# Optimization experiments

Hardware: AMD Instinct MI355X
Metric: run time of the kernel (lower is better)

## Reference

```python
import jax, jax.numpy as jnp
import numpy as np

H = 64          # hidden_size
NG = 5000       # num_genes
B = 32          # num_graphs
N = B * NG      # total nodes
E = 1_600_000   # total edges


def setup_inputs() -> dict:
    key = jax.random.key(0)
    ks = jax.random.split(key, 32)
    def nrm(k, shape, s=0.05):
        return jax.random.normal(k, shape, jnp.float32) * s
    return {
        "x": jax.random.normal(ks[0], (N, 2), jnp.float32),
        "edge_index": jax.random.randint(ks[1], (2, E), 0, N),
        # pert_w: Linear(1, H); gene_basal_w: Linear(1, H)
        "pert_w_W": nrm(ks[2], (H, 1)), "pert_w_b": nrm(ks[3], (H,)),
        "basal_W": nrm(ks[4], (H, 1)), "basal_b": nrm(ks[5], (H,)),
        # gene embedding table (max_norm=True -> rows renormed to norm<=1)
        "emb_table": nrm(ks[6], (NG, H), 0.5),
        # emb_trans: Linear(2H, H)
        "emb_trans_W": nrm(ks[7], (H, 2 * H)), "emb_trans_b": nrm(ks[8], (H,)),
        # pert_base_trans_w: Linear(2H, H)  (gene_pert_agg == 'concat+w')
        "pbt_W": nrm(ks[9], (H, 2 * H)), "pbt_b": nrm(ks[10], (H,)),
        # two GCNConv(H, H) layers
        "gcn1_W": nrm(ks[11], (H, H)), "gcn1_b": nrm(ks[12], (H,)),
        "gcn2_W": nrm(ks[13], (H, H)), "gcn2_b": nrm(ks[14], (H,)),
        # recovery_w: MLP([H, 2H, H, 1]) with BN on first two hidden layers
        "rec_W1": nrm(ks[15], (2 * H, H)), "rec_b1": nrm(ks[16], (2 * H,)),
        "rec_g1": jnp.ones((2 * H,), jnp.float32), "rec_be1": jnp.zeros((2 * H,), jnp.float32),
        "rec_W2": nrm(ks[17], (H, 2 * H)), "rec_b2": nrm(ks[18], (H,)),
        "rec_g2": jnp.ones((H,), jnp.float32), "rec_be2": jnp.zeros((H,), jnp.float32),
        "rec_W3": nrm(ks[19], (1, H)), "rec_b3": nrm(ks[20], (1,)),
    }


def _gcn_conv(h, src, dst, norm, W, b, n_nodes):
    # PyG GCNConv: x' = scatter_add(norm * (x W^T)[src] -> dst) + b, self-loops included in src/dst
    m = h @ W.T                                   # [N, H]
    out = jax.ops.segment_sum(m[src] * norm[:, None], dst, num_segments=n_nodes)
    return out + b


def _batchnorm(z, g, b, eps=1e-5):
    mu = z.mean(0)
    var = z.var(0)
    return (z - mu) * jax.lax.rsqrt(var + eps) * g + b


def reference(x, edge_index, pert_w_W, pert_w_b, basal_W, basal_b, emb_table,
              emb_trans_W, emb_trans_b, pbt_W, pbt_b, gcn1_W, gcn1_b,
              gcn2_W, gcn2_b, rec_W1, rec_b1, rec_g1, rec_be1,
              rec_W2, rec_b2, rec_g2, rec_be2, rec_W3, rec_b3):
    n_nodes = x.shape[0]
    ng = emb_table.shape[0]
    nb = n_nodes // ng

    # GCN normalization with self-loops (computed once, shared by both layers)
    loop = jnp.arange(n_nodes)
    src = jnp.concatenate([edge_index[0], loop])
    dst = jnp.concatenate([edge_index[1], loop])
    deg = jax.ops.segment_sum(jnp.ones_like(src, jnp.float32), dst, num_segments=n_nodes)
    dinv = jnp.where(deg > 0, jax.lax.rsqrt(jnp.maximum(deg, 1.0)), 0.0)
    norm = dinv[src] * dinv[dst]

    pert_emb = x[:, 1:2] @ pert_w_W.T + pert_w_b          # [N, H]
    base = x[:, 0:1] @ basal_W.T + basal_b                # [N, H]

    # nn.Embedding(max_norm=True): renorm rows to max L2 norm of 1
    nrm = jnp.linalg.norm(emb_table, axis=1, keepdims=True)
    emb_n = emb_table * jnp.minimum(1.0, 1.0 / jnp.maximum(nrm, 1e-7))
    emb = jnp.tile(emb_n, (nb, 1))                        # arange(NG).repeat(B) lookup
    base_emb = jnp.concatenate([emb, base], axis=1) @ emb_trans_W.T + emb_trans_b

    def pbt(p, b_):
        return jnp.concatenate([p, b_], axis=1) @ pbt_W.T + pbt_b

    h = pbt(pert_emb, base_emb)
    h = pbt(jax.nn.relu(_gcn_conv(h, src, dst, norm, gcn1_W, gcn1_b, n_nodes)), base_emb)
    h = pbt(jax.nn.relu(_gcn_conv(h, src, dst, norm, gcn2_W, gcn2_b, n_nodes)), base_emb)

    # recovery_w: Linear -> BN -> ReLU -> Linear -> BN -> ReLU -> Linear
    z = jax.nn.relu(_batchnorm(h @ rec_W1.T + rec_b1, rec_g1, rec_be1))
    z = jax.nn.relu(_batchnorm(z @ rec_W2.T + rec_b2, rec_g2, rec_be2))
    out = z @ rec_W3.T + rec_b3                           # [N, 1]
    return out.reshape(nb, ng)
```

## Files before the change

### kernel.cpp

```cpp
#include <hip/hip_runtime.h>


#define GS_GRID 2048
#define GS_BLK  256

enum { A1_=0, A0_=64, C1_=128, C0_=192, D1_=256, D0_=320,
       S1_=384, Q1_=512, SC1_=640, SH1_=768,
       S2_=896, Q2_=960, SC2_=1024, SH2_=1088,
       GD1_=1152, GA1_=1216, G00_=1280,
       GD2_=1344, G02_=1408, RD1_=1472, RD0_=1600, CST_FLOATS=2048 };

__device__ __forceinline__ float wave_sum64(float v) {
#pragma unroll
  for (int o = 32; o; o >>= 1) v += __shfl_xor(v, o, 64);
  return v;
}

__device__ __forceinline__ int rfl(int v) { return __builtin_amdgcn_readfirstlane(v); }

__device__ __forceinline__ float rlane(float v, int k) {
  return __int_as_float(__builtin_amdgcn_readlane(__float_as_int(v), k));
}


__global__ __launch_bounds__(256) void hist_k(const int* __restrict__ ei,
                                              int* __restrict__ hist, int E) {
  __shared__ int h[256];
  const int t = threadIdx.x;
  h[t] = 0;
  __syncthreads();
  const int per = (E + gridDim.x - 1) / gridDim.x;
  const int beg = blockIdx.x * per, end = min(E, beg + per);
  for (int i = beg + t; i < end; i += 256)
    atomicAdd(&h[ei[E + i] >> 10], 1);
  __syncthreads();
  hist[blockIdx.x * 256 + t] = h[t];
}

__global__ void bscan_k(int* __restrict__ hist, int* __restrict__ bucketBase,
                        int* __restrict__ rowptrN, int E, int nblk) {
  const int t = threadIdx.x;
  int run = 0;
  for (int b = 0; b < nblk; ++b) {
    int v = hist[b * 256 + t];
    hist[b * 256 + t] = run;
    run += v;
  }
  __shared__ int sc[256];
  sc[t] = run; __syncthreads();
  for (int o = 1; o < 256; o <<= 1) {
    int x = sc[t]; if (t >= o) x += sc[t - o];
    __syncthreads(); sc[t] = x; __syncthreads();
  }
  bucketBase[t] = sc[t] - run;
  if (t == 255) { bucketBase[256] = sc[t]; rowptrN[0] = E; }
}

__global__ __launch_bounds__(256) void bucket_k(const int* __restrict__ ei,
                                                const int* __restrict__ hist,
                                                const int* __restrict__ bucketBase,
                                                int2* __restrict__ eb, int E) {
  __shared__ int cur[256];
  const int t = threadIdx.x;
  cur[t] = hist[blockIdx.x * 256 + t] + bucketBase[t];
  __syncthreads();
  const int per = (E + gridDim.x - 1) / gridDim.x;
  const int beg = blockIdx.x * per, end = min(E, beg + per);
  for (int i = beg + t; i < end; i += 256) {
    int s = ei[i], d = ei[E + i];
    int pos = atomicAdd(&cur[d >> 10], 1);
    eb[pos] = make_int2(s, d);
  }
}

__global__ __launch_bounds__(256) void csr_k(const int2* __restrict__ eb,
                                             const int* __restrict__ bucketBase,
                                             int* __restrict__ rowptr, float* __restrict__ dinv,
                                             int* __restrict__ col, int N) {
  __shared__ int cnt[1024];
  __shared__ int base[1024];
  __shared__ int red[256];
  const int t = threadIdx.x;
  const int k = blockIdx.x;
  const int nodeBeg = k << 10;
  const int segBeg = bucketBase[k], segEnd = bucketBase[k + 1];
#pragma unroll
  for (int j = t; j < 1024; j += 256) cnt[j] = 0;
  __syncthreads();
  for (int i = segBeg + t; i < segEnd; i += 256)
    atomicAdd(&cnt[eb[i].y & 1023], 1);
  __syncthreads();
  int c0 = cnt[4 * t], c1 = cnt[4 * t + 1], c2 = cnt[4 * t + 2], c3 = cnt[4 * t + 3];
  int ts = c0 + c1 + c2 + c3;
  red[t] = ts; __syncthreads();
  for (int o = 1; o < 256; o <<= 1) {
    int x = red[t]; if (t >= o) x += red[t - o];
    __syncthreads(); red[t] = x; __syncthreads();
  }
  int off = red[t] - ts;
  base[4 * t] = off;
  base[4 * t + 1] = off + c0;
  base[4 * t + 2] = off + c0 + c1;
  base[4 * t + 3] = off + c0 + c1 + c2;
#pragma unroll
  for (int u = 0; u < 4; ++u) {
    int j = 4 * t + u;
    int node = nodeBeg + j;
    if (node < N) {
      rowptr[node] = segBeg + base[j];
      dinv[node] = rsqrtf((float)(cnt[j] + 1));
    }
  }
  __syncthreads();
  cnt[4 * t] = base[4 * t]; cnt[4 * t + 1] = base[4 * t + 1];
  cnt[4 * t + 2] = base[4 * t + 2]; cnt[4 * t + 3] = base[4 * t + 3];
  __syncthreads();
  for (int i = segBeg + t; i < segEnd; i += 256) {
    int2 e = eb[i];
    int pos = atomicAdd(&cnt[e.y & 1023], 1);
    col[segBeg + pos] = e.x;
  }
}

__global__ void consts1_k(const float* __restrict__ pbtW, const float* __restrict__ pertW,
                          const float* __restrict__ pertB, const float* __restrict__ etW,
                          const float* __restrict__ basW, const float* __restrict__ basB,
                          const float* __restrict__ etB, float* __restrict__ cst) {
  int h = threadIdx.x;
  float a1 = 0, a0 = 0, c1 = 0, c0 = 0;
  for (int k = 0; k < 64; ++k) {
    float wp = pbtW[h * 128 + k];
    a1 = fmaf(wp, pertW[k], a1);
    a0 = fmaf(wp, pertB[k], a0);
    float we = etW[h * 128 + 64 + k];
    c1 = fmaf(we, basW[k], c1);
    c0 = fmaf(we, basB[k], c0);
  }
  cst[A1_ + h] = a1; cst[A0_ + h] = a0; cst[C1_ + h] = c1; cst[C0_ + h] = c0 + etB[h];
}

__global__ void consts2_k(const float* __restrict__ pbtW, const float* __restrict__ pbtB,
                          float* __restrict__ cst) {
  int h = threadIdx.x;
  float d1 = 0, d0 = 0;
  for (int k = 0; k < 64; ++k) {
    float w = pbtW[h * 128 + 64 + k];
    d1 = fmaf(w, cst[C1_ + k], d1);
    d0 = fmaf(w, cst[C0_ + k], d0);
  }
  cst[D1_ + h] = d1; cst[D0_ + h] = d0 + pbtB[h];
}

__global__ void consts3_k(const float* __restrict__ g1W, float* __restrict__ cst) {
  int h = threadIdx.x;
  float gd1 = 0, ga1 = 0, g00 = 0;
  for (int k = 0; k < 64; ++k) {
    float w = g1W[h * 64 + k];
    gd1 = fmaf(w, cst[D1_ + k], gd1);
    ga1 = fmaf(w, cst[A1_ + k], ga1);
    g00 = fmaf(w, cst[D0_ + k] + cst[A0_ + k], g00);
  }
  cst[GD1_ + h] = gd1; cst[GA1_ + h] = ga1; cst[G00_ + h] = g00;
}

__global__ void consts5_k(const float* __restrict__ g2W, float* __restrict__ cst) {
  int h = threadIdx.x;
  float a = 0, b = 0;
  for (int k = 0; k < 64; ++k) {
    float w = g2W[h * 64 + k];
    a = fmaf(w, cst[D1_ + k], a);
    b = fmaf(w, cst[D0_ + k], b);
  }
  cst[GD2_ + h] = a; cst[G02_ + h] = b;
}

__global__ void consts6_k(const float* __restrict__ rW1, const float* __restrict__ rb1,
                          float* __restrict__ cst) {
  int c = threadIdx.x;
  float a = 0, b = 0;
  for (int k = 0; k < 64; ++k) {
    float w = rW1[c * 64 + k];
    a = fmaf(w, cst[D1_ + k], a);
    b = fmaf(w, cst[D0_ + k], b);
  }
  cst[RD1_ + c] = a; cst[RD0_ + c] = b + rb1[c];
}

__global__ void constsW_k(const float* __restrict__ g2W, const float* __restrict__ rW1,
                          const float* __restrict__ pbtW,
                          float* __restrict__ Wf, float* __restrict__ Wr) {
  const int t = threadIdx.x;
  for (int e = t; e < 4096; e += 256) {
    int c = e >> 6, j = e & 63;
    float s = 0.f;
    for (int h = 0; h < 64; ++h) s = fmaf(g2W[c * 64 + h], pbtW[h * 128 + j], s);
    Wf[e] = s;
  }
  for (int e = t; e < 8192; e += 256) {
    int c = e >> 6, j = e & 63;
    float s = 0.f;
    for (int h = 0; h < 64; ++h) s = fmaf(rW1[c * 64 + h], pbtW[h * 128 + j], s);
    Wr[e] = s;
  }
}

template <bool NORM>
__global__ __launch_bounds__(256) void geneT_k(const float* __restrict__ in,
                                               const float* __restrict__ W, int ldw,
                                               float* __restrict__ out, int NG) {
  const int lane = threadIdx.x & 63;
  const int wid = blockIdx.x * 4 + (threadIdx.x >> 6);
  const int nw = gridDim.x * 4;
  float w[64];
#pragma unroll
  for (int j = 0; j < 16; ++j) {
    float4 v = *reinterpret_cast<const float4*>(W + lane * ldw + 4 * j);
    w[4 * j] = v.x; w[4 * j + 1] = v.y; w[4 * j + 2] = v.z; w[4 * j + 3] = v.w;
  }
  for (int g = wid; g < NG; g += nw) {
    float e = in[g * 64 + lane];
    if (NORM) {
      float sq = wave_sum64(e * e);
      float nrm = sqrtf(sq);
      float s = nrm > 1.f ? 1.f / nrm : 1.f;
      e *= s;
    }
    float acc = 0.f;
#pragma unroll
    for (int k = 0; k < 64; ++k) acc = fmaf(w[k], rlane(e, k), acc);
    out[g * 64 + lane] = acc;
  }
}

__global__ __launch_bounds__(256) void m1_k(const float* __restrict__ x,
                                            const float* __restrict__ embTm1,
                                            const float* __restrict__ dinv,
                                            const float* __restrict__ cst,
                                            float* __restrict__ m1, int N, int NG) {
  int total = N * 16;
  for (int idx = blockIdx.x * blockDim.x + threadIdx.x; idx < total;
       idx += gridDim.x * blockDim.x) {
    int n = idx >> 4, q = idx & 15;
    int g = n % NG;
    float x0 = x[2 * n], x1 = x[2 * n + 1], dn = dinv[n];
    float4 em = *reinterpret_cast<const float4*>(embTm1 + g * 64 + q * 4);
    float4 gd1 = *reinterpret_cast<const float4*>(cst + GD1_ + q * 4);
    float4 ga1 = *reinterpret_cast<const float4*>(cst + GA1_ + q * 4);
    float4 g00 = *reinterpret_cast<const float4*>(cst + G00_ + q * 4);
    float4 mv;
    mv.x = dn * (fmaf(x0, gd1.x, fmaf(x1, ga1.x, em.x + g00.x)));
    mv.y = dn * (fmaf(x0, gd1.y, fmaf(x1, ga1.y, em.y + g00.y)));
    mv.z = dn * (fmaf(x0, gd1.z, fmaf(x1, ga1.z, em.z + g00.z)));
    mv.w = dn * (fmaf(x0, gd1.w, fmaf(x1, ga1.w, em.w + g00.w)));
    reinterpret_cast<float4*>(m1)[idx] = mv;
  }
}

#define XS_STRIDE 130
#define WS_STRIDE 68
#define OS_STRIDE 68
#define OS_WORDS  (128 * OS_STRIDE)
#define WS_WORDS  (64 * WS_STRIDE)
#define LDS_WORDS (OS_WORDS + WS_WORDS + 128)

template <bool MUL_D, bool STATS>
__global__ __launch_bounds__(256, 4) void gemmt_gv_k(
    const float* __restrict__ in,
    const float* __restrict__ W,
    const float* __restrict__ tbl,
    const float* __restrict__ cA,
    const float* __restrict__ cB,
    const float* __restrict__ x,
    const float* __restrict__ dinv,
    float* __restrict__ out, int ldout,
    float* __restrict__ sums, float* __restrict__ sqs, int N, int NG) {
  __shared__ float lds[LDS_WORDS];
  float* Xs = lds;
  float* Ws = lds + OS_WORDS;
  float* sred = lds + OS_WORDS + WS_WORDS;
  const int t = threadIdx.x;
  const int base = blockIdx.x << 7;
  if (STATS && t < 128) sred[t] = 0.f;

#pragma unroll
  for (int c = 0; c < 16; ++c) {
    int lin = c * 256 + t;
    int cw = lin >> 6, kw = lin & 63;
    Ws[kw * WS_STRIDE + cw] = W[cw * 64 + kw];
  }
#pragma unroll
  for (int c = 0; c < 8; ++c) {
    int lin = c * 256 + t;
    int nl = lin >> 4, k4 = lin & 15;
    int row = base + nl; if (row >= N) row = N - 1;
    float4 v = *reinterpret_cast<const float4*>(in + (size_t)row * 64 + 4 * k4);
    Xs[(4 * k4 + 0) * XS_STRIDE + nl] = v.x;
    Xs[(4 * k4 + 1) * XS_STRIDE + nl] = v.y;
    Xs[(4 * k4 + 2) * XS_STRIDE + nl] = v.z;
    Xs[(4 * k4 + 3) * XS_STRIDE + nl] = v.w;
  }
  __syncthreads();

  const int ng = t & 31;
  const int c0 = (t >> 5) * 8;
  float acc[8][4];
#pragma unroll
  for (int i = 0; i < 8; ++i)
#pragma unroll
    for (int j = 0; j < 4; ++j) acc[i][j] = 0.f;
#pragma unroll 4
  for (int k = 0; k < 64; ++k) {
    float4 wa = *reinterpret_cast<const float4*>(Ws + k * WS_STRIDE + c0);
    float4 wb = *reinterpret_cast<const float4*>(Ws + k * WS_STRIDE + c0 + 4);
    float2 xa = *reinterpret_cast<const float2*>(Xs + k * XS_STRIDE + 2 * ng);
    float2 xb = *reinterpret_cast<const float2*>(Xs + k * XS_STRIDE + 2 * ng + 64);
    const float w8[8] = {wa.x, wa.y, wa.z, wa.w, wb.x, wb.y, wb.z, wb.w};
    const float x4[4] = {xa.x, xa.y, xb.x, xb.y};
#pragma unroll
    for (int ci = 0; ci < 8; ++ci)
#pragma unroll
      for (int xi = 0; xi < 4; ++xi)
        acc[ci][xi] = fmaf(w8[ci], x4[xi], acc[ci][xi]);
  }
  __syncthreads();

  const int nd[4] = {2 * ng, 2 * ng + 1, 2 * ng + 64, 2 * ng + 65};
#pragma unroll
  for (int ci = 0; ci < 8; ++ci) {
    Xs[nd[0] * OS_STRIDE + c0 + ci] = acc[ci][0];
    Xs[nd[1] * OS_STRIDE + c0 + ci] = acc[ci][1];
    Xs[nd[2] * OS_STRIDE + c0 + ci] = acc[ci][2];
    Xs[nd[3] * OS_STRIDE + c0 + ci] = acc[ci][3];
  }
  __syncthreads();

  const int q = t & 15;
  const float4 a4 = *reinterpret_cast<const float4*>(cA + 4 * q);
  const float4 b4 = *reinterpret_cast<const float4*>(cB + 4 * q);
  float4 s4 = make_float4(0.f, 0.f, 0.f, 0.f);
  float4 q4 = make_float4(0.f, 0.f, 0.f, 0.f);
#pragma unroll
  for (int c = 0; c < 8; ++c) {
    int nl = c * 16 + (t >> 4);
    int n = base + nl;
    if (n < N) {
      float4 o = *reinterpret_cast<const float4*>(Xs + nl * OS_STRIDE + 4 * q);
      int g = n % NG;
      float4 tg = *reinterpret_cast<const float4*>(tbl + (size_t)g * 64 + 4 * q);
      float x0 = x[2 * n];
      o.x += fmaf(x0, a4.x, tg.x + b4.x);
      o.y += fmaf(x0, a4.y, tg.y + b4.y);
      o.z += fmaf(x0, a4.z, tg.z + b4.z);
      o.w += fmaf(x0, a4.w, tg.w + b4.w);
      if (MUL_D) {
        float dv = dinv[n];
        o.x *= dv; o.y *= dv; o.z *= dv; o.w *= dv;
      }
      *reinterpret_cast<float4*>(out + (size_t)n * ldout + 4 * q) = o;
      if (STATS) {
        s4.x += o.x; s4.y += o.y; s4.z += o.z; s4.w += o.w;
        q4.x += o.x * o.x; q4.y += o.y * o.y; q4.z += o.z * o.z; q4.w += o.w * o.w;
      }
    }
  }
  if (STATS) {
    atomicAdd(&sred[4 * q + 0], s4.x);
    atomicAdd(&sred[4 * q + 1], s4.y);
    atomicAdd(&sred[4 * q + 2], s4.z);
    atomicAdd(&sred[4 * q + 3], s4.w);
    atomicAdd(&sred[64 + 4 * q + 0], q4.x);
    atomicAdd(&sred[64 + 4 * q + 1], q4.y);
    atomicAdd(&sred[64 + 4 * q + 2], q4.z);
    atomicAdd(&sred[64 + 4 * q + 3], q4.w);
    __syncthreads();
    if (t < 64) {
      atomicAdd(&sums[t], sred[t]);
      atomicAdd(&sqs[t], sred[64 + t]);
    }
  }
}

__global__ __launch_bounds__(256, 4) void gemmt_rec2_k(
    const float* __restrict__ Z,
    const float* __restrict__ W,
    const float* __restrict__ b,
    const float* __restrict__ bnsc, const float* __restrict__ bnsh,
    float* __restrict__ out,
    float* __restrict__ sums, float* __restrict__ sqs, int N) {
  __shared__ float lds[LDS_WORDS];
  float* Xs = lds;
  float* Ws = lds + OS_WORDS;
  float* sred = lds + OS_WORDS + WS_WORDS;
  const int t = threadIdx.x;
  const int base = blockIdx.x << 7;
  if (t < 128) sred[t] = 0.f;

  const int ng = t & 31;
  const int c0 = (t >> 5) * 8;
  float acc[8][4];
#pragma unroll
  for (int i = 0; i < 8; ++i)
#pragma unroll
    for (int j = 0; j < 4; ++j) acc[i][j] = 0.f;

  for (int half = 0; half < 2; ++half) {
    if (half) __syncthreads();
    const int ko = half * 64;
#pragma unroll
    for (int c = 0; c < 16; ++c) {
      int lin = c * 256 + t;
      int cw = lin >> 6, kw = lin & 63;
      Ws[kw * WS_STRIDE + cw] = W[cw * 128 + ko + kw];
    }
#pragma unroll
    for (int c = 0; c < 8; ++c) {
      int lin = c * 256 + t;
      int nl = lin >> 4, k4 = lin & 15;
      int row = base + nl; if (row >= N) row = N - 1;
      float4 v = *reinterpret_cast<const float4*>(Z + (size_t)row * 128 + ko + 4 * k4);
      float4 sc = *reinterpret_cast<const float4*>(bnsc + ko + 4 * k4);
      float4 sh = *reinterpret_cast<const float4*>(bnsh + ko + 4 * k4);
      v.x = fmaxf(fmaf(v.x, sc.x, sh.x), 0.f);
      v.y = fmaxf(fmaf(v.y, sc.y, sh.y), 0.f);
      v.z = fmaxf(fmaf(v.z, sc.z, sh.z), 0.f);
      v.w = fmaxf(fmaf(v.w, sc.w, sh.w), 0.f);
      Xs[(4 * k4 + 0) * XS_STRIDE + nl] = v.x;
      Xs[(4 * k4 + 1) * XS_STRIDE + nl] = v.y;
      Xs[(4 * k4 + 2) * XS_STRIDE + nl] = v.z;
      Xs[(4 * k4 + 3) * XS_STRIDE + nl] = v.w;
    }
    __syncthreads();
#pragma unroll 4
    for (int k = 0; k < 64; ++k) {
      float4 wa = *reinterpret_cast<const float4*>(Ws + k * WS_STRIDE + c0);
      float4 wb = *reinterpret_cast<const float4*>(Ws + k * WS_STRIDE + c0 + 4);
      float2 xa = *reinterpret_cast<const float2*>(Xs + k * XS_STRIDE + 2 * ng);
      float2 xb = *reinterpret_cast<const float2*>(Xs + k * XS_STRIDE + 2 * ng + 64);
      const float w8[8] = {wa.x, wa.y, wa.z, wa.w, wb.x, wb.y, wb.z, wb.w};
      const float x4[4] = {xa.x, xa.y, xb.x, xb.y};
#pragma unroll
      for (int ci = 0; ci < 8; ++ci)
#pragma unroll
        for (int xi = 0; xi < 4; ++xi)
          acc[ci][xi] = fmaf(w8[ci], x4[xi], acc[ci][xi]);
    }
  }
  __syncthreads();

  const int nd[4] = {2 * ng, 2 * ng + 1, 2 * ng + 64, 2 * ng + 65};
#pragma unroll
  for (int ci = 0; ci < 8; ++ci) {
    Xs[nd[0] * OS_STRIDE + c0 + ci] = acc[ci][0];
    Xs[nd[1] * OS_STRIDE + c0 + ci] = acc[ci][1];
    Xs[nd[2] * OS_STRIDE + c0 + ci] = acc[ci][2];
    Xs[nd[3] * OS_STRIDE + c0 + ci] = acc[ci][3];
  }
  __syncthreads();

  const int q = t & 15;
  const float4 bb = *reinterpret_cast<const float4*>(b + 4 * q);
  float4 s4 = make_float4(0.f, 0.f, 0.f, 0.f);
  float4 q4 = make_float4(0.f, 0.f, 0.f, 0.f);
#pragma unroll
  for (int c = 0; c < 8; ++c) {
    int nl = c * 16 + (t >> 4);
    int n = base + nl;
    if (n < N) {
      float4 o = *reinterpret_cast<const float4*>(Xs + nl * OS_STRIDE + 4 * q);
      o.x += bb.x; o.y += bb.y; o.z += bb.z; o.w += bb.w;
      *reinterpret_cast<float4*>(out + (size_t)n * 64 + 4 * q) = o;
      s4.x += o.x; s4.y += o.y; s4.z += o.z; s4.w += o.w;
      q4.x += o.x * o.x; q4.y += o.y * o.y; q4.z += o.z * o.z; q4.w += o.w * o.w;
    }
  }
  atomicAdd(&sred[4 * q + 0], s4.x);
  atomicAdd(&sred[4 * q + 1], s4.y);
  atomicAdd(&sred[4 * q + 2], s4.z);
  atomicAdd(&sred[4 * q + 3], s4.w);
  atomicAdd(&sred[64 + 4 * q + 0], q4.x);
  atomicAdd(&sred[64 + 4 * q + 1], q4.y);
  atomicAdd(&sred[64 + 4 * q + 2], q4.z);
  atomicAdd(&sred[64 + 4 * q + 3], q4.w);
  __syncthreads();
  if (t < 64) {
    atomicAdd(&sums[t], sred[t]);
    atomicAdd(&sqs[t], sred[64 + t]);
  }
}

__global__ __launch_bounds__(256) void gather_k(const float* __restrict__ m,
                                                const int* __restrict__ rowptr,
                                                const int* __restrict__ col,
                                                const float* __restrict__ dinv,
                                                const float* __restrict__ bias,
                                                float* __restrict__ out, int N) {
  const int lane = threadIdx.x & 63;
  const int wid = blockIdx.x * 4 + (threadIdx.x >> 6);
  const int nw = gridDim.x * 4;
  const float b = bias[lane];
  for (int n = wid; n < N; n += nw) {
    const int nn = rfl(n);
    const float dn = dinv[nn];
    float acc = m[(size_t)nn * 64 + lane];
    float acc2 = 0.f;
    const int beg = rfl(rowptr[nn]), end = rfl(rowptr[nn + 1]);
    for (int base = beg; base < end; base += 64) {
      const int rem = end - base;
      const int kk = rem < 64 ? rem : 64;
      int cv = (lane < kk) ? col[base + lane] : 0;
      int k = 0;
      for (; k + 3 < kk; k += 4) {
        int i0 = __shfl(cv, k, 64), i1 = __shfl(cv, k + 1, 64);
        int i2 = __shfl(cv, k + 2, 64), i3 = __shfl(cv, k + 3, 64);
        float v0 = m[(size_t)i0 * 64 + lane];
        float v1 = m[(size_t)i1 * 64 + lane];
        float v2 = m[(size_t)i2 * 64 + lane];
        float v3 = m[(size_t)i3 * 64 + lane];
        acc += v0 + v2; acc2 += v1 + v3;
      }
      for (; k < kk; ++k) acc += m[(size_t)__shfl(cv, k, 64) * 64 + lane];
    }
    out[(size_t)nn * 64 + lane] = fmaxf(fmaf(dn, acc + acc2, b), 0.f);
  }
}

__global__ void bnparam_k(const float* __restrict__ sums, const float* __restrict__ sqs,
                          const float* __restrict__ g, const float* __restrict__ be,
                          float* __restrict__ scale, float* __restrict__ shift, int C,
                          float invN) {
  int t = threadIdx.x;
  if (t < C) {
    float mu = sums[t] * invN;
    float var = fmaxf(sqs[t] * invN - mu * mu, 0.f);
    float sc = g[t] * rsqrtf(var + 1e-5f);
    scale[t] = sc;
    shift[t] = be[t] - mu * sc;
  }
}

__global__ __launch_bounds__(256) void rec3_k(const float* __restrict__ z2,
                                              const float* __restrict__ scale,
                                              const float* __restrict__ shift,
                                              const float* __restrict__ W3,
                                              const float* __restrict__ b3,
                                              float* __restrict__ out, int N) {
  const int lane = threadIdx.x & 63;
  const int wid = blockIdx.x * 4 + (threadIdx.x >> 6);
  const int nw = gridDim.x * 4;
  const float sc = scale[lane], sh = shift[lane], w = W3[lane], b = b3[0];
  for (int n = wid; n < N; n += nw) {
    float v = z2[(size_t)n * 64 + lane];
    v = fmaxf(fmaf(v, sc, sh), 0.f) * w;
    v = wave_sum64(v);
    if (lane == 0) out[n] = v + b;
  }
}

extern "C" void kernel_launch(void* const* d_in, const int* in_sizes, int n_in,
                              void* d_out, int out_size, void* d_ws, size_t ws_size,
                              hipStream_t stream) {
  const float* x     = (const float*)d_in[0];
  const int*   ei    = (const int*)d_in[1];
  const float* pertW = (const float*)d_in[2];
  const float* pertB = (const float*)d_in[3];
  const float* basW  = (const float*)d_in[4];
  const float* basB  = (const float*)d_in[5];
  const float* embTb = (const float*)d_in[6];
  const float* etW   = (const float*)d_in[7];
  const float* etB   = (const float*)d_in[8];
  const float* pbtW  = (const float*)d_in[9];
  const float* pbtB  = (const float*)d_in[10];
  const float* g1W   = (const float*)d_in[11];
  const float* g1B   = (const float*)d_in[12];
  const float* g2W   = (const float*)d_in[13];
  const float* g2B   = (const float*)d_in[14];
  const float* rW1   = (const float*)d_in[15];
  const float* rb1   = (const float*)d_in[16];
  const float* rg1   = (const float*)d_in[17];
  const float* rbe1  = (const float*)d_in[18];
  const float* rW2   = (const float*)d_in[19];
  const float* rb2   = (const float*)d_in[20];
  const float* rg2   = (const float*)d_in[21];
  const float* rbe2  = (const float*)d_in[22];
  const float* rW3   = (const float*)d_in[23];
  const float* rb3   = (const float*)d_in[24];
  float* outp = (float*)d_out;

  const int N  = in_sizes[0] / 2;
  const int E  = in_sizes[1] / 2;
  const int NG = in_sizes[6] / 64;
  const int NB = (N + 1023) >> 10;
  const int NT = (N + 127) >> 7;

  char* p = (char*)d_ws;
  float* cst    = (float*)p; p += CST_FLOATS * 4;
  int*   hist   = (int*)p;   p += 256 * 256 * 4;
  int*   bb     = (int*)p;   p += 1024;
  int*   rowptr = (int*)p;   p += (size_t)(N + 64) * 4;
  float* dinv   = (float*)p; p += (size_t)N * 4;
  int*   col    = (int*)p;   p += (size_t)E * 4;
  float* Wf     = (float*)p; p += 4096 * 4;
  float* Wr     = (float*)p; p += 8192 * 4;
  float* embT   = (float*)p; p += (size_t)NG * 64 * 4;
  float* embT2  = (float*)p; p += (size_t)NG * 64 * 4;
  float* embT2g2= (float*)p; p += (size_t)NG * 64 * 4;
  float* embT2rA= (float*)p; p += (size_t)NG * 64 * 4;
  float* embT2rB= (float*)p; p += (size_t)NG * 64 * 4;
  float* z2buf  = (float*)p; p += (size_t)N * 64 * 4;
  float* hb     = (float*)p; p += (size_t)N * 64 * 4;
  float* tmp1   = (float*)p; p += (size_t)N * 64 * 4;
  float* tmp2   = (float*)p; p += (size_t)N * 64 * 4;
  float* Z = hb;
  float* z2 = z2buf;
  float* embTm1 = embT;
  int2*  eb = (int2*)tmp2;

  dim3 blk(GS_BLK), grid(GS_GRID);

  hipMemsetAsync(cst, 0, CST_FLOATS * 4, stream);

  hist_k<<<256, 256, 0, stream>>>(ei, hist, E);
  bscan_k<<<1, 256, 0, stream>>>(hist, bb, rowptr + N, E, 256);
  bucket_k<<<256, 256, 0, stream>>>(ei, hist, bb, eb, E);
  csr_k<<<NB, 256, 0, stream>>>(eb, bb, rowptr, dinv, col, N);

  consts1_k<<<1, 64, 0, stream>>>(pbtW, pertW, pertB, etW, basW, basB, etB, cst);
  consts2_k<<<1, 64, 0, stream>>>(pbtW, pbtB, cst);
  consts3_k<<<1, 64, 0, stream>>>(g1W, cst);
  consts5_k<<<1, 64, 0, stream>>>(g2W, cst);
  consts6_k<<<1, 128, 0, stream>>>(rW1, rb1, cst);
  constsW_k<<<1, 256, 0, stream>>>(g2W, rW1, pbtW, Wf, Wr);
  geneT_k<true><<<256, 256, 0, stream>>>(embTb, etW, 128, embT, NG);
  geneT_k<false><<<256, 256, 0, stream>>>(embT, pbtW + 64, 128, embT2, NG);
  geneT_k<false><<<256, 256, 0, stream>>>(embT2, g1W, 64, embTm1, NG);
  geneT_k<false><<<256, 256, 0, stream>>>(embT2, g2W, 64, embT2g2, NG);
  geneT_k<false><<<256, 256, 0, stream>>>(embT2, rW1, 64, embT2rA, NG);
  geneT_k<false><<<256, 256, 0, stream>>>(embT2, rW1 + 64 * 64, 64, embT2rB, NG);
  m1_k<<<grid, blk, 0, stream>>>(x, embTm1, dinv, cst, tmp1, N, NG);

  gather_k<<<grid, blk, 0, stream>>>(tmp1, rowptr, col, dinv, g1B, tmp2, N);
  gemmt_gv_k<true, false><<<NT, blk, 0, stream>>>(
      tmp2, Wf, embT2g2, cst + GD2_, cst + G02_, x, dinv, tmp1, 64,
      nullptr, nullptr, N, NG);
  gather_k<<<grid, blk, 0, stream>>>(tmp1, rowptr, col, dinv, g2B, tmp2, N);

  gemmt_gv_k<false, true><<<NT, blk, 0, stream>>>(
      tmp2, Wr, embT2rA, cst + RD1_, cst + RD0_, x, nullptr, Z, 128,
      cst + S1_, cst + Q1_, N, NG);
  gemmt_gv_k<false, true><<<NT, blk, 0, stream>>>(
      tmp2, Wr + 64 * 64, embT2rB, cst + RD1_ + 64, cst + RD0_ + 64, x, nullptr,
      Z + 64, 128, cst + S1_ + 64, cst + Q1_ + 64, N, NG);
  bnparam_k<<<1, 128, 0, stream>>>(cst + S1_, cst + Q1_, rg1, rbe1,
                                   cst + SC1_, cst + SH1_, 128, 1.0f / (float)N);
  gemmt_rec2_k<<<NT, blk, 0, stream>>>(Z, rW2, rb2, cst + SC1_, cst + SH1_,
                                       z2, cst + S2_, cst + Q2_, N);
  bnparam_k<<<1, 64, 0, stream>>>(cst + S2_, cst + Q2_, rg2, rbe2,
                                  cst + SC2_, cst + SH2_, 64, 1.0f / (float)N);
  rec3_k<<<grid, blk, 0, stream>>>(z2, cst + SC2_, cst + SH2_, rW3, rb3, outp, N);
}
```

Baseline: 569.2 us.

## Parallelize bucket scan, fuse rec1 GEMM halves, unroll gather by eight

Replaces the single-block serial histogram scan with a two-stage parallel scan: 256 blocks, each scanning one bucket column, then a small scan over the bucket totals. Merges the two recovery-layer-1 GEMM launches into one kernel that loads the input tile once and computes both 64-column halves with two accumulator sets. Widens the gather inner loop to eight independent loads with four partial sums to expose more memory-level parallelism. The cost is higher register pressure in the fused GEMM and the gather, which may lower occupancy.

Result: faster. 485.9 us (-14.6%).

```diff
diff --git a/kernel.cpp b/kernel.cpp
--- a/kernel.cpp
+++ b/kernel.cpp
@@ -37,22 +37,31 @@
   hist[blockIdx.x * 256 + t] = h[t];
 }
 
-__global__ void bscan_k(int* __restrict__ hist, int* __restrict__ bucketBase,
-                        int* __restrict__ rowptrN, int E, int nblk) {
+__global__ void scan1b_k(int* __restrict__ hist, int* __restrict__ bsum) {
+  __shared__ int sc[256];
   const int t = threadIdx.x;
-  int run = 0;
-  for (int b = 0; b < nblk; ++b) {
-    int v = hist[b * 256 + t];
-    hist[b * 256 + t] = run;
-    run += v;
-  }
-  __shared__ int sc[256];
-  sc[t] = run; __syncthreads();
+  const int b = blockIdx.x;
+  int v = hist[t * 256 + b];
+  sc[t] = v; __syncthreads();
   for (int o = 1; o < 256; o <<= 1) {
     int x = sc[t]; if (t >= o) x += sc[t - o];
     __syncthreads(); sc[t] = x; __syncthreads();
   }
-  bucketBase[t] = sc[t] - run;
+  hist[t * 256 + b] = sc[t] - v;
+  if (t == 255) bsum[b] = sc[t];
+}
+
+__global__ void scan2b_k(const int* __restrict__ bsum, int* __restrict__ bucketBase,
+                         int* __restrict__ rowptrN, int E) {
+  __shared__ int sc[256];
+  const int t = threadIdx.x;
+  int v = bsum[t];
+  sc[t] = v; __syncthreads();
+  for (int o = 1; o < 256; o <<= 1) {
+    int x = sc[t]; if (t >= o) x += sc[t - o];
+    __syncthreads(); sc[t] = x; __syncthreads();
+  }
+  bucketBase[t] = sc[t] - v;
   if (t == 255) { bucketBase[256] = sc[t]; rowptrN[0] = E; }
 }
 
@@ -263,7 +272,7 @@
 #define WS_WORDS  (64 * WS_STRIDE)
 #define LDS_WORDS (OS_WORDS + WS_WORDS + 128)
 
-template <bool MUL_D, bool STATS>
+template <bool MUL_D>
 __global__ __launch_bounds__(256, 4) void gemmt_gv_k(
     const float* __restrict__ in,
     const float* __restrict__ W,
@@ -272,15 +281,12 @@
     const float* __restrict__ cB,
     const float* __restrict__ x,
     const float* __restrict__ dinv,
-    float* __restrict__ out, int ldout,
-    float* __restrict__ sums, float* __restrict__ sqs, int N, int NG) {
+    float* __restrict__ out, int ldout, int N, int NG) {
   __shared__ float lds[LDS_WORDS];
   float* Xs = lds;
   float* Ws = lds + OS_WORDS;
-  float* sred = lds + OS_WORDS + WS_WORDS;
   const int t = threadIdx.x;
   const int base = blockIdx.x << 7;
-  if (STATS && t < 128) sred[t] = 0.f;
 
 #pragma unroll
   for (int c = 0; c < 16; ++c) {
@@ -337,8 +343,6 @@
   const int q = t & 15;
   const float4 a4 = *reinterpret_cast<const float4*>(cA + 4 * q);
   const float4 b4 = *reinterpret_cast<const float4*>(cB + 4 * q);
-  float4 s4 = make_float4(0.f, 0.f, 0.f, 0.f);
-  float4 q4 = make_float4(0.f, 0.f, 0.f, 0.f);
 #pragma unroll
   for (int c = 0; c < 8; ++c) {
     int nl = c * 16 + (t >> 4);
@@ -357,26 +361,181 @@
         o.x *= dv; o.y *= dv; o.z *= dv; o.w *= dv;
       }
       *reinterpret_cast<float4*>(out + (size_t)n * ldout + 4 * q) = o;
-      if (STATS) {
+    }
+  }
+}
+
+__global__ __launch_bounds__(256, 4) void gemmt_rec1_k(
+    const float* __restrict__ in,
+    const float* __restrict__ Wr,
+    const float* __restrict__ tblA, const float* __restrict__ tblB,
+    const float* __restrict__ cA,
+    const float* __restrict__ cB,
+    const float* __restrict__ x,
+    float* __restrict__ Z,
+    float* __restrict__ sums, float* __restrict__ sqs,
+    int N, int NG) {
+  __shared__ float lds[LDS_WORDS];
+  float* Xs = lds;
+  float* Ws = lds + OS_WORDS;
+  float* sred = lds + OS_WORDS + WS_WORDS;
+  const int t = threadIdx.x;
+  const int base = blockIdx.x << 7;
+  if (t < 128) sred[t] = 0.f;
+
+#pragma unroll
+  for (int c = 0; c < 16; ++c) {
+    int lin = c * 256 + t;
+    int cw = lin >> 6, kw = lin & 63;
+    Ws[kw * WS_STRIDE + cw] = Wr[cw * 64 + kw];
+  }
+#pragma unroll
+  for (int c = 0; c < 8; ++c) {
+    int lin = c * 256 + t;
+    int nl = lin >> 4, k4 = lin & 15;
+    int row = base + nl; if (row >= N) row = N - 1;
+    float4 v = *reinterpret_cast<const float4*>(in + (size_t)row * 64 + 4 * k4);
+    Xs[(4 * k4 + 0) * XS_STRIDE + nl] = v.x;
+    Xs[(4 * k4 + 1) * XS_STRIDE + nl] = v.y;
+    Xs[(4 * k4 + 2) * XS_STRIDE + nl] = v.z;
+    Xs[(4 * k4 + 3) * XS_STRIDE + nl] = v.w;
+  }
+  __syncthreads();
+
+  const int ng = t & 31;
+  const int c0 = (t >> 5) * 8;
+  float accA[8][4], accB[8][4];
+#pragma unroll
+  for (int i = 0; i < 8; ++i)
+#pragma unroll
+    for (int j = 0; j < 4; ++j) { accA[i][j] = 0.f; accB[i][j] = 0.f; }
+
+#pragma unroll 4
+  for (int k = 0; k < 64; ++k) {
+    float4 wa = *reinterpret_cast<const float4*>(Ws + k * WS_STRIDE + c0);
+    float4 wb = *reinterpret_cast<const float4*>(Ws + k * WS_STRIDE + c0 + 4);
+    float2 xa = *reinterpret_cast<const float2*>(Xs + k * XS_STRIDE + 2 * ng);
+    float2 xb = *reinterpret_cast<const float2*>(Xs + k * XS_STRIDE + 2 * ng + 64);
+    const float w8[8] = {wa.x, wa.y, wa.z, wa.w, wb.x, wb.y, wb.z, wb.w};
+    const float x4[4] = {xa.x, xa.y, xb.x, xb.y};
+#pragma unroll
+    for (int ci = 0; ci < 8; ++ci)
+#pragma unroll
+      for (int xi = 0; xi < 4; ++xi)
+        accA[ci][xi] = fmaf(w8[ci], x4[xi], accA[ci][xi]);
+  }
+  __syncthreads();
+#pragma unroll
+  for (int c = 0; c < 16; ++c) {
+    int lin = c * 256 + t;
+    int cw = lin >> 6, kw = lin & 63;
+    Ws[kw * WS_STRIDE + cw] = Wr[(64 + cw) * 64 + kw];
+  }
+  __syncthreads();
+#pragma unroll 4
+  for (int k = 0; k < 64; ++k) {
+    float4 wa = *reinterpret_cast<const float4*>(Ws + k * WS_STRIDE + c0);
+    float4 wb = *reinterpret_cast<const float4*>(Ws + k * WS_STRIDE + c0 + 4);
+    float2 xa = *reinterpret_cast<const float2*>(Xs + k * XS_STRIDE + 2 * ng);
+    float2 xb = *reinterpret_cast<const float2*>(Xs + k * XS_STRIDE + 2 * ng + 64);
+    const float w8[8] = {wa.x, wa.y, wa.z, wa.w, wb.x, wb.y, wb.z, wb.w};
+    const float x4[4] = {xa.x, xa.y, xb.x, xb.y};
+#pragma unroll
+    for (int ci = 0; ci < 8; ++ci)
+#pragma unroll
+      for (int xi = 0; xi < 4; ++xi)
+        accB[ci][xi] = fmaf(w8[ci], x4[xi], accB[ci][xi]);
+  }
+  __syncthreads();
+
+  const int nd[4] = {2 * ng, 2 * ng + 1, 2 * ng + 64, 2 * ng + 65};
+  const int q = t & 15;
+
+#pragma unroll
+  for (int ci = 0; ci < 8; ++ci) {
+    Xs[nd[0] * OS_STRIDE + c0 + ci] = accA[ci][0];
+    Xs[nd[1] * OS_STRIDE + c0 + ci] = accA[ci][1];
+    Xs[nd[2] * OS_STRIDE + c0 + ci] = accA[ci][2];
+    Xs[nd[3] * OS_STRIDE + c0 + ci] = accA[ci][3];
+  }
+  __syncthreads();
+  {
+    const float4 a4 = *reinterpret_cast<const float4*>(cA + 4 * q);
+    const float4 b4 = *reinterpret_cast<const float4*>(cB + 4 * q);
+    float4 s4 = make_float4(0.f, 0.f, 0.f, 0.f);
+    float4 q4 = make_float4(0.f, 0.f, 0.f, 0.f);
+#pragma unroll
+    for (int c = 0; c < 8; ++c) {
+      int nl = c * 16 + (t >> 4);
+      int n = base + nl;
+      if (n < N) {
+        float4 o = *reinterpret_cast<const float4*>(Xs + nl * OS_STRIDE + 4 * q);
+        int g = n % NG;
+        float4 tg = *reinterpret_cast<const float4*>(tblA + (size_t)g * 64 + 4 * q);
+        float x0 = x[2 * n];
+        o.x += fmaf(x0, a4.x, tg.x + b4.x);
+        o.y += fmaf(x0, a4.y, tg.y + b4.y);
+        o.z += fmaf(x0, a4.z, tg.z + b4.z);
+        o.w += fmaf(x0, a4.w, tg.w + b4.w);
+        *reinterpret_cast<float4*>(Z + (size_t)n * 128 + 4 * q) = o;
         s4.x += o.x; s4.y += o.y; s4.z += o.z; s4.w += o.w;
         q4.x += o.x * o.x; q4.y += o.y * o.y; q4.z += o.z * o.z; q4.w += o.w * o.w;
       }
     }
-  }
-  if (STATS) {
-    atomicAdd(&sred[4 * q + 0], s4.x);
-    atomicAdd(&sred[4 * q + 1], s4.y);
-    atomicAdd(&sred[4 * q + 2], s4.z);
-    atomicAdd(&sred[4 * q + 3], s4.w);
-    atomicAdd(&sred[64 + 4 * q + 0], q4.x);
-    atomicAdd(&sred[64 + 4 * q + 1], q4.y);
-    atomicAdd(&sred[64 + 4 * q + 2], q4.z);
-    atomicAdd(&sred[64 + 4 * q + 3], q4.w);
-    __syncthreads();
-    if (t < 64) {
-      atomicAdd(&sums[t], sred[t]);
-      atomicAdd(&sqs[t], sred[64 + t]);
-    }
+    atomicAdd(&sred[4 * q + 0], s4.x); atomicAdd(&sred[4 * q + 1], s4.y);
+    atomicAdd(&sred[4 * q + 2], s4.z); atomicAdd(&sred[4 * q + 3], s4.w);
+    atomicAdd(&sred[64 + 4 * q + 0], q4.x); atomicAdd(&sred[64 + 4 * q + 1], q4.y);
+    atomicAdd(&sred[64 + 4 * q + 2], q4.z); atomicAdd(&sred[64 + 4 * q + 3], q4.w);
+  }
+  __syncthreads();
+  if (t < 64) {
+    atomicAdd(&sums[t], sred[t]);
+    atomicAdd(&sqs[t], sred[64 + t]);
+  }
+  __syncthreads();
+  if (t < 128) sred[t] = 0.f;
+  __syncthreads();
+
+#pragma unroll
+  for (int ci = 0; ci < 8; ++ci) {
+    Xs[nd[0] * OS_STRIDE + c0 + ci] = accB[ci][0];
+    Xs[nd[1] * OS_STRIDE + c0 + ci] = accB[ci][1];
+    Xs[nd[2] * OS_STRIDE + c0 + ci] = accB[ci][2];
+    Xs[nd[3] * OS_STRIDE + c0 + ci] = accB[ci][3];
+  }
+  __syncthreads();
+  {
+    const float4 a4 = *reinterpret_cast<const float4*>(cA + 64 + 4 * q);
+    const float4 b4 = *reinterpret_cast<const float4*>(cB + 64 + 4 * q);
+    float4 s4 = make_float4(0.f, 0.f, 0.f, 0.f);
+    float4 q4 = make_float4(0.f, 0.f, 0.f, 0.f);
+#pragma unroll
+    for (int c = 0; c < 8; ++c) {
+      int nl = c * 16 + (t >> 4);
+      int n = base + nl;
+      if (n < N) {
+        float4 o = *reinterpret_cast<const float4*>(Xs + nl * OS_STRIDE + 4 * q);
+        int g = n % NG;
+        float4 tg = *reinterpret_cast<const float4*>(tblB + (size_t)g * 64 + 4 * q);
+        float x0 = x[2 * n];
+        o.x += fmaf(x0, a4.x, tg.x + b4.x);
+        o.y += fmaf(x0, a4.y, tg.y + b4.y);
+        o.z += fmaf(x0, a4.z, tg.z + b4.z);
+        o.w += fmaf(x0, a4.w, tg.w + b4.w);
+        *reinterpret_cast<float4*>(Z + (size_t)n * 128 + 64 + 4 * q) = o;
+        s4.x += o.x; s4.y += o.y; s4.z += o.z; s4.w += o.w;
+        q4.x += o.x * o.x; q4.y += o.y * o.y; q4.z += o.z * o.z; q4.w += o.w * o.w;
+      }
+    }
+    atomicAdd(&sred[4 * q + 0], s4.x); atomicAdd(&sred[4 * q + 1], s4.y);
+    atomicAdd(&sred[4 * q + 2], s4.z); atomicAdd(&sred[4 * q + 3], s4.w);
+    atomicAdd(&sred[64 + 4 * q + 0], q4.x); atomicAdd(&sred[64 + 4 * q + 1], q4.y);
+    atomicAdd(&sred[64 + 4 * q + 2], q4.z); atomicAdd(&sred[64 + 4 * q + 3], q4.w);
+  }
+  __syncthreads();
+  if (t < 64) {
+    atomicAdd(&sums[64 + t], sred[t]);
+    atomicAdd(&sqs[64 + t], sred[64 + t]);
   }
 }
 
@@ -473,14 +632,10 @@
       q4.x += o.x * o.x; q4.y += o.y * o.y; q4.z += o.z * o.z; q4.w += o.w * o.w;
     }
   }
-  atomicAdd(&sred[4 * q + 0], s4.x);
-  atomicAdd(&sred[4 * q + 1], s4.y);
-  atomicAdd(&sred[4 * q + 2], s4.z);
-  atomicAdd(&sred[4 * q + 3], s4.w);
-  atomicAdd(&sred[64 + 4 * q + 0], q4.x);
-  atomicAdd(&sred[64 + 4 * q + 1], q4.y);
-  atomicAdd(&sred[64 + 4 * q + 2], q4.z);
-  atomicAdd(&sred[64 + 4 * q + 3], q4.w);
+  atomicAdd(&sred[4 * q + 0], s4.x); atomicAdd(&sred[4 * q + 1], s4.y);
+  atomicAdd(&sred[4 * q + 2], s4.z); atomicAdd(&sred[4 * q + 3], s4.w);
+  atomicAdd(&sred[64 + 4 * q + 0], q4.x); atomicAdd(&sred[64 + 4 * q + 1], q4.y);
+  atomicAdd(&sred[64 + 4 * q + 2], q4.z); atomicAdd(&sred[64 + 4 * q + 3], q4.w);
   __syncthreads();
   if (t < 64) {
     atomicAdd(&sums[t], sred[t]);
@@ -501,26 +656,39 @@
   for (int n = wid; n < N; n += nw) {
     const int nn = rfl(n);
     const float dn = dinv[nn];
-    float acc = m[(size_t)nn * 64 + lane];
-    float acc2 = 0.f;
+    float a0 = m[(size_t)nn * 64 + lane];
+    float a1 = 0.f, a2 = 0.f, a3 = 0.f;
     const int beg = rfl(rowptr[nn]), end = rfl(rowptr[nn + 1]);
     for (int base = beg; base < end; base += 64) {
       const int rem = end - base;
       const int kk = rem < 64 ? rem : 64;
       int cv = (lane < kk) ? col[base + lane] : 0;
       int k = 0;
-      for (; k + 3 < kk; k += 4) {
-        int i0 = __shfl(cv, k, 64), i1 = __shfl(cv, k + 1, 64);
+      for (; k + 7 < kk; k += 8) {
+        int i0 = __shfl(cv, k, 64),     i1 = __shfl(cv, k + 1, 64);
         int i2 = __shfl(cv, k + 2, 64), i3 = __shfl(cv, k + 3, 64);
+        int i4 = __shfl(cv, k + 4, 64), i5 = __shfl(cv, k + 5, 64);
+        int i6 = __shfl(cv, k + 6, 64), i7 = __shfl(cv, k + 7, 64);
         float v0 = m[(size_t)i0 * 64 + lane];
         float v1 = m[(size_t)i1 * 64 + lane];
         float v2 = m[(size_t)i2 * 64 + lane];
         float v3 = m[(size_t)i3 * 64 + lane];
-        acc += v0 + v2; acc2 += v1 + v3;
+        float v4 = m[(size_t)i4 * 64 + lane];
+        float v5 = m[(size_t)i5 * 64 + lane];
+        float v6 = m[(size_t)i6 * 64 + lane];
+        float v7 = m[(size_t)i7 * 64 + lane];
+        a0 += v0 + v4; a1 += v1 + v5; a2 += v2 + v6; a3 += v3 + v7;
       }
-      for (; k < kk; ++k) acc += m[(size_t)__shfl(cv, k, 64) * 64 + lane];
-    }
-    out[(size_t)nn * 64 + lane] = fmaxf(fmaf(dn, acc + acc2, b), 0.f);
+      for (; k + 1 < kk; k += 2) {
+        int i0 = __shfl(cv, k, 64), i1 = __shfl(cv, k + 1, 64);
+        float v0 = m[(size_t)i0 * 64 + lane];
+        float v1 = m[(size_t)i1 * 64 + lane];
+        a0 += v0; a1 += v1;
+      }
+      if (k < kk) a0 += m[(size_t)__shfl(cv, k, 64) * 64 + lane];
+    }
+    float acc = (a0 + a1) + (a2 + a3);
+    out[(size_t)nn * 64 + lane] = fmaxf(fmaf(dn, acc, b), 0.f);
   }
 }
 
@@ -596,6 +764,7 @@
   float* cst    = (float*)p; p += CST_FLOATS * 4;
   int*   hist   = (int*)p;   p += 256 * 256 * 4;
   int*   bb     = (int*)p;   p += 1024;
+  int*   bsum   = (int*)p;   p += 1024;
   int*   rowptr = (int*)p;   p += (size_t)(N + 64) * 4;
   float* dinv   = (float*)p; p += (size_t)N * 4;
   int*   col    = (int*)p;   p += (size_t)E * 4;
@@ -620,7 +789,8 @@
   hipMemsetAsync(cst, 0, CST_FLOATS * 4, stream);
 
   hist_k<<<256, 256, 0, stream>>>(ei, hist, E);
-  bscan_k<<<1, 256, 0, stream>>>(hist, bb, rowptr + N, E, 256);
+  scan1b_k<<<256, 256, 0, stream>>>(hist, bsum);
+  scan2b_k<<<1, 256, 0, stream>>>(bsum, bb, rowptr + N, E);
   bucket_k<<<256, 256, 0, stream>>>(ei, hist, bb, eb, E);
   csr_k<<<NB, 256, 0, stream>>>(eb, bb, rowptr, dinv, col, N);
 
@@ -639,17 +809,13 @@
   m1_k<<<grid, blk, 0, stream>>>(x, embTm1, dinv, cst, tmp1, N, NG);
 
   gather_k<<<grid, blk, 0, stream>>>(tmp1, rowptr, col, dinv, g1B, tmp2, N);
-  gemmt_gv_k<true, false><<<NT, blk, 0, stream>>>(
-      tmp2, Wf, embT2g2, cst + GD2_, cst + G02_, x, dinv, tmp1, 64,
-      nullptr, nullptr, N, NG);
+  gemmt_gv_k<true><<<NT, blk, 0, stream>>>(
+      tmp2, Wf, embT2g2, cst + GD2_, cst + G02_, x, dinv, tmp1, 64, N, NG);
   gather_k<<<grid, blk, 0, stream>>>(tmp1, rowptr, col, dinv, g2B, tmp2, N);
 
-  gemmt_gv_k<false, true><<<NT, blk, 0, stream>>>(
-      tmp2, Wr, embT2rA, cst + RD1_, cst + RD0_, x, nullptr, Z, 128,
+  gemmt_rec1_k<<<NT, blk, 0, stream>>>(
+      tmp2, Wr, embT2rA, embT2rB, cst + RD1_, cst + RD0_, x, Z,
       cst + S1_, cst + Q1_, N, NG);
-  gemmt_gv_k<false, true><<<NT, blk, 0, stream>>>(
-      tmp2, Wr + 64 * 64, embT2rB, cst + RD1_ + 64, cst + RD0_ + 64, x, nullptr,
-      Z + 64, 128, cst + S1_ + 64, cst + Q1_ + 64, N, NG);
   bnparam_k<<<1, 128, 0, stream>>>(cst + S1_, cst + Q1_, rg1, rbe1,
                                    cst + SC1_, cst + SH1_, 128, 1.0f / (float)N);
   gemmt_rec2_k<<<NT, blk, 0, stream>>>(Z, rW2, rb2, cst + SC1_, cst + SH1_,
```
